# Kernel tuning notes

Hardware: AMD Instinct MI355X
Metric: run time of the kernel (lower is better)

Reference implementation:

```python
import jax, jax.numpy as jnp
import numpy as np
from jax import lax

IN_CH = 256
NUM_CLASSES = 21
ROI = 7
SCALE = 1.0 / 32
SR = 2  # sampling_ratio
B = 2
NPROP = 128
FH = FW = 32
IMG = 1024
SCORE_THRESH = 0.05
NMS_THRESH = 0.5
MAX_DET = 100


def setup_inputs() -> dict:
    key = jax.random.key(0)
    ks = jax.random.split(key, 10)
    features = jax.random.normal(ks[0], (B, IN_CH, FH, FW), jnp.float32)
    x1 = jax.random.uniform(ks[1], (B, NPROP), minval=0.0, maxval=IMG - 160.0)
    y1 = jax.random.uniform(ks[2], (B, NPROP), minval=0.0, maxval=IMG - 160.0)
    w = jax.random.uniform(ks[3], (B, NPROP), minval=32.0, maxval=160.0)
    h = jax.random.uniform(ks[4], (B, NPROP), minval=32.0, maxval=160.0)
    proposals = jnp.stack([x1, y1, x1 + w, y1 + h], axis=-1)  # [B, NPROP, 4]
    img_sizes = jnp.full((B, 2), IMG, dtype=jnp.int32)  # (h, w)
    feat_dim = IN_CH * ROI * ROI

    def kaiming(k, shape):
        return jax.random.normal(k, shape, jnp.float32) * np.float32(np.sqrt(2.0 / shape[1]))

    W1 = kaiming(ks[5], (1024, feat_dim)); b1 = jnp.zeros((1024,), jnp.float32)
    W2 = kaiming(ks[6], (1024, 1024)); b2 = jnp.zeros((1024,), jnp.float32)
    Wc = jax.random.normal(ks[7], (NUM_CLASSES, 1024), jnp.float32) * 0.01
    bc = jnp.zeros((NUM_CLASSES,), jnp.float32)
    Wb = jax.random.normal(ks[8], (NUM_CLASSES * 4, 1024), jnp.float32) * 0.001
    bb = jnp.zeros((NUM_CLASSES * 4,), jnp.float32)
    return dict(features=features, proposals=proposals, img_sizes=img_sizes,
                W1=W1, b1=b1, W2=W2, b2=b2, Wc=Wc, bc=bc, Wb=Wb, bb=bb)


def roi_align(features, bidx, rois):
    """torchvision-style RoIAlign (aligned=False), spatial_scale=SCALE, sampling_ratio=SR.
    features [B,C,H,W], bidx [N] int, rois [N,4] -> [N, C*ROI*ROI] (channel-major flatten)."""
    Bf, C, H, W = features.shape
    x1 = rois[:, 0] * SCALE; y1 = rois[:, 1] * SCALE
    x2 = rois[:, 2] * SCALE; y2 = rois[:, 3] * SCALE
    rw = jnp.maximum(x2 - x1, 1.0); rh = jnp.maximum(y2 - y1, 1.0)
    bw = rw / ROI; bh = rh / ROI
    # per-bin sample offsets: [ROI, SR]
    g = jnp.arange(ROI, dtype=jnp.float32)[:, None] + (jnp.arange(SR, dtype=jnp.float32)[None, :] + 0.5) / SR
    ys = y1[:, None, None] + g[None] * bh[:, None, None]  # [N, ROI, SR]
    xs = x1[:, None, None] + g[None] * bw[:, None, None]  # [N, ROI, SR]
    y = ys[:, :, :, None, None]  # [N,ph,sy,1,1]
    x = xs[:, None, None, :, :]  # [N,1,1,pw,sx]
    inb = (y >= -1.0) & (y <= H) & (x >= -1.0) & (x <= W)  # [N,ph,sy,pw,sx]
    yc = jnp.clip(y, 0.0, H - 1.0); xc = jnp.clip(x, 0.0, W - 1.0)
    y0f = jnp.floor(yc); x0f = jnp.floor(xc)
    y0 = y0f.astype(jnp.int32); x0 = x0f.astype(jnp.int32)
    y1i = jnp.minimum(y0 + 1, H - 1); x1i = jnp.minimum(x0 + 1, W - 1)
    ly = yc - y0f; lx = xc - x0f
    hy = 1.0 - ly; hx = 1.0 - lx
    b = bidx[:, None, None, None, None]
    # gather four corners: advanced indices broadcast -> [N,ph,sy,pw,sx,C]
    f00 = features[b, :, y0, x0]
    f01 = features[b, :, y0, x1i]
    f10 = features[b, :, y1i, x0]
    f11 = features[b, :, y1i, x1i]
    val = ((hy * hx)[..., None] * f00 + (hy * lx)[..., None] * f01
           + (ly * hx)[..., None] * f10 + (ly * lx)[..., None] * f11)
    val = val * inb[..., None]
    pooled = val.mean(axis=(2, 4))            # [N, ph, pw, C]
    pooled = jnp.transpose(pooled, (0, 3, 1, 2))  # [N, C, ph, pw] (torch layout)
    return pooled.reshape(pooled.shape[0], -1)


def decode_boxes(deltas, props):
    pw = props[..., 2] - props[..., 0]
    ph = props[..., 3] - props[..., 1]
    px = props[..., 0] + pw / 2
    py = props[..., 1] + ph / 2
    cx = px + deltas[..., 0] * pw
    cy = py + deltas[..., 1] * ph
    w = pw * jnp.exp(deltas[..., 2])
    h = ph * jnp.exp(deltas[..., 3])
    return jnp.stack([cx - w / 2, cy - h / 2, cx + w / 2, cy + h / 2], axis=-1)


def nms_fixed(boxes, scores, valid, iou_thresh, max_out):
    """Greedy NMS with fixed shapes. Returns (indices[max_out], ok_mask[max_out])."""
    M = scores.shape[0]
    s = jnp.where(valid, scores, -jnp.inf)
    order = jnp.argsort(-s)
    b = boxes[order]; v = valid[order]
    bx1, by1, bx2, by2 = b[:, 0], b[:, 1], b[:, 2], b[:, 3]
    area = (bx2 - bx1) * (by2 - by1)
    idxs = jnp.arange(M)

    def body(i, keep):
        xi1 = jnp.maximum(bx1[i], bx1); yi1 = jnp.maximum(by1[i], by1)
        xi2 = jnp.minimum(bx2[i], bx2); yi2 = jnp.minimum(by2[i], by2)
        inter = jnp.maximum(xi2 - xi1, 0.0) * jnp.maximum(yi2 - yi1, 0.0)
        iou = inter / (area[i] + area - inter + 1e-9)
        suppress = (iou > iou_thresh) & (idxs > i)
        return jnp.where(keep[i], keep & ~suppress, keep)

    keep = lax.fori_loop(0, M, body, v)
    pos = jnp.where(keep, idxs, M)
    take = jnp.sort(pos)[:max_out]
    ok = take < M
    take = jnp.where(ok, take, 0)
    return order[take], ok


def postprocess_image(probs, reg, props, img_hw):
    Ncls = probs.shape[1]
    scores = probs[:, 1:]                    # [N, C-1] (skip background)
    deltas = reg[:, 1:, :]                   # [N, C-1, 4]
    boxes = decode_boxes(deltas, props[:, None, :])  # [N, C-1, 4]
    h = img_hw[0].astype(boxes.dtype); w = img_hw[1].astype(boxes.dtype)
    boxes = jnp.stack([jnp.clip(boxes[..., 0], 0.0, w), jnp.clip(boxes[..., 1], 0.0, h),
                       jnp.clip(boxes[..., 2], 0.0, w), jnp.clip(boxes[..., 3], 0.0, h)], axis=-1)
    labels = jnp.broadcast_to(jnp.arange(1, Ncls, dtype=jnp.int32)[None, :], scores.shape)
    fb = boxes.reshape(-1, 4); fs = scores.reshape(-1); fl = labels.reshape(-1)
    valid = fs > SCORE_THRESH
    maxc = jnp.max(jnp.where(valid, jnp.max(fb, axis=1), 0.0))
    off = fl.astype(fb.dtype) * (maxc + 1.0)
    zero = jnp.zeros_like(off)
    fb_off = fb + jnp.stack([off, zero, off, zero], axis=-1)
    idx, ok = nms_fixed(fb_off, fs, valid, NMS_THRESH, MAX_DET)
    m = ok.astype(fb.dtype)
    return fb[idx] * m[:, None], fs[idx] * m, fl[idx] * ok.astype(jnp.int32)


def reference(features, proposals, img_sizes, W1, b1, W2, b2, Wc, bc, Wb, bb):
    Bn, NP = proposals.shape[0], proposals.shape[1]
    bidx = jnp.repeat(jnp.arange(Bn, dtype=jnp.int32), NP)
    props_flat = proposals.reshape(-1, 4)
    roi_feats = roi_align(features, bidx, props_flat)       # [N, C*49]
    x = jax.nn.relu(roi_feats @ W1.T + b1)
    x = jax.nn.relu(x @ W2.T + b2)
    cls_logits = x @ Wc.T + bc                              # [N, NUM_CLASSES]
    box_reg = (x @ Wb.T + bb).reshape(-1, NUM_CLASSES, 4)   # [N, NUM_CLASSES, 4]
    probs = jax.nn.softmax(cls_logits, axis=-1)
    out_b, out_s, out_l = [], [], []
    for i in range(Bn):
        p = probs[i * NP:(i + 1) * NP]
        r = box_reg[i * NP:(i + 1) * NP]
        bi, si, li = postprocess_image(p, r, proposals[i], img_sizes[i])
        out_b.append(bi); out_s.append(si); out_l.append(li)
    return jnp.stack(out_b), jnp.stack(out_s), jnp.stack(out_l)
```

## Files before the change

kernel.cpp:

```cpp
#include <hip/hip_runtime.h>
#include <math.h>

#define IN_CH   256
#define NCLS    21
#define ROIW    7
#define NPROP   128
#define BATCH   2
#define NROI    (BATCH*NPROP)
#define FEAT_DIM (IN_CH*ROIW*ROIW)
#define HID     1024
#define NCAND   (NPROP*(NCLS-1))
#define MAXDET  100
#define SCORE_T 0.05f
#define NMS_T   0.5f
#define SPLIT1  32

__global__ __launch_bounds__(256) void transpose_feat(const float* __restrict__ feat,
                                                      float* __restrict__ ft) {
    int img = blockIdx.z;
    int cb = blockIdx.y;
    int pb = blockIdx.x;
    __shared__ float t[32][33];
    int tx = threadIdx.x & 31, ty = threadIdx.x >> 5;
#pragma unroll
    for (int i = 0; i < 4; ++i) {
        int c = ty + i * 8;
        t[c][tx] = feat[(size_t)img * 262144 + (size_t)(cb * 32 + c) * 1024 + pb * 32 + tx];
    }
    __syncthreads();
#pragma unroll
    for (int i = 0; i < 4; ++i) {
        int p = ty + i * 8;
        ft[(size_t)img * 262144 + (size_t)(pb * 32 + p) * 256 + cb * 32 + tx] = t[tx][p];
    }
}

__global__ __launch_bounds__(256) void roi_align_tr(const float* __restrict__ ft,
                                                    const float* __restrict__ props,
                                                    float* __restrict__ out) {
    int n = blockIdx.x >> 1;
    int half = blockIdx.x & 1;
    int img = n / NPROP;
    int q0 = half ? 25 : 0;
    int nq = half ? 24 : 25;
    const float* pr = props + n * 4;
    float x1 = pr[0] * 0.03125f, y1 = pr[1] * 0.03125f;
    float x2 = pr[2] * 0.03125f, y2 = pr[3] * 0.03125f;
    float rw = fmaxf(x2 - x1, 1.0f), rh = fmaxf(y2 - y1, 1.0f);
    float bw = rw / 7.0f, bh = rh / 7.0f;
    int cg = threadIdx.x & 63;
    int qg = threadIdx.x >> 6;
    __shared__ float tile[25][260];
    const float* base = ft + (size_t)img * 262144 + cg * 4;
    for (int j = qg; j < nq; j += 4) {
        int q = q0 + j;
        int iy = q / 7, ix = q % 7;
        float ax = 0.f, ay = 0.f, az = 0.f, aw = 0.f;
#pragma unroll
        for (int s = 0; s < 4; ++s) {
            int sy = s >> 1, sx = s & 1;
            float gy = (float)iy + ((float)sy + 0.5f) / 2.0f;
            float gx = (float)ix + ((float)sx + 0.5f) / 2.0f;
            float y = y1 + gy * bh;
            float x = x1 + gx * bw;
            bool inb = (y >= -1.0f) && (y <= 32.0f) && (x >= -1.0f) && (x <= 32.0f);
            float yc = fminf(fmaxf(y, 0.0f), 31.0f);
            float xc = fminf(fmaxf(x, 0.0f), 31.0f);
            float y0f = floorf(yc), x0f = floorf(xc);
            int y0 = (int)y0f, x0i = (int)x0f;
            int y1i = min(y0 + 1, 31), x1i = min(x0i + 1, 31);
            float ly = yc - y0f, lx = xc - x0f;
            float hy = 1.0f - ly, hx = 1.0f - lx;
            float wg = inb ? 1.0f : 0.0f;
            float w00 = hy * hx * wg, w01 = hy * lx * wg, w10 = ly * hx * wg, w11 = ly * lx * wg;
            float4 f00 = *(const float4*)(base + (size_t)(y0 * 32 + x0i) * 256);
            float4 f01 = *(const float4*)(base + (size_t)(y0 * 32 + x1i) * 256);
            float4 f10 = *(const float4*)(base + (size_t)(y1i * 32 + x0i) * 256);
            float4 f11 = *(const float4*)(base + (size_t)(y1i * 32 + x1i) * 256);
            ax += w00 * f00.x + w01 * f01.x + w10 * f10.x + w11 * f11.x;
            ay += w00 * f00.y + w01 * f01.y + w10 * f10.y + w11 * f11.y;
            az += w00 * f00.z + w01 * f01.z + w10 * f10.z + w11 * f11.z;
            aw += w00 * f00.w + w01 * f01.w + w10 * f10.w + w11 * f11.w;
        }
        *(float4*)&tile[j][cg * 4] = make_float4(ax * 0.25f, ay * 0.25f, az * 0.25f, aw * 0.25f);
    }
    __syncthreads();
    float* ob = out + (size_t)n * FEAT_DIM + q0;
    int tid = threadIdx.x;
    if (half == 0) {
        for (int i = tid; i < 256 * 25; i += 256) {
            int c = i / 25, ql = i % 25;
            ob[c * 49 + ql] = tile[ql][c];
        }
    } else {
        for (int i = tid; i < 256 * 24; i += 256) {
            int c = i / 24, ql = i % 24;
            ob[c * 49 + ql] = tile[ql][c];
        }
    }
}

#define GBM 128
#define GBN 128
#define GBK 8
__global__ __launch_bounds__(256, 2) void gemm_tn_part(const float* __restrict__ A,
                                                       const float* __restrict__ Wt,
                                                       float* __restrict__ Cp,
                                                       int Nr, int Mo, int K) {
    const int S = gridDim.z;
    const int kchunk = K / S;
    const int k0 = blockIdx.z * kchunk;
    const int n0 = blockIdx.y * GBM;
    const int j0 = blockIdx.x * GBN;
    __shared__ float As[GBK][GBM + 4];
    __shared__ float Ws[GBK][GBN + 4];
    const int tid = threadIdx.x;
    const int tx = tid & 15;
    const int ty = tid >> 4;
    const int r0 = ty << 2;
    const int c0 = tx << 2;
    const int srow = tid >> 1;
    const int skk  = (tid & 1) << 2;
    float acc[8][8];
#pragma unroll
    for (int r = 0; r < 8; ++r)
#pragma unroll
        for (int c = 0; c < 8; ++c) acc[r][c] = 0.0f;

    const int iters = kchunk / GBK;
    const float* Abase = A + (size_t)(n0 + srow) * K + skk;
    const float* Wbase = Wt + (size_t)(j0 + srow) * K + skk;
    float4 pa = *(const float4*)(Abase + k0);
    float4 pw = *(const float4*)(Wbase + k0);

#pragma unroll 1
    for (int it = 0; it < iters; ++it) {
        __syncthreads();
        As[skk + 0][srow] = pa.x; As[skk + 1][srow] = pa.y;
        As[skk + 2][srow] = pa.z; As[skk + 3][srow] = pa.w;
        Ws[skk + 0][srow] = pw.x; Ws[skk + 1][srow] = pw.y;
        Ws[skk + 2][srow] = pw.z; Ws[skk + 3][srow] = pw.w;
        __syncthreads();
        if (it + 1 < iters) {
            int kc = k0 + (it + 1) * GBK;
            pa = *(const float4*)(Abase + kc);
            pw = *(const float4*)(Wbase + kc);
        }
        float4 fa0[2], fa1[2], fw0[2], fw1[2];
        fa0[0] = *(const float4*)&As[0][r0];
        fa1[0] = *(const float4*)&As[0][r0 + 64];
        fw0[0] = *(const float4*)&Ws[0][c0];
        fw1[0] = *(const float4*)&Ws[0][c0 + 64];
#pragma unroll
        for (int k = 0; k < GBK; ++k) {
            const int cur = k & 1, nxt = cur ^ 1;
            if (k + 1 < GBK) {
                fa0[nxt] = *(const float4*)&As[k + 1][r0];
                fa1[nxt] = *(const float4*)&As[k + 1][r0 + 64];
                fw0[nxt] = *(const float4*)&Ws[k + 1][c0];
                fw1[nxt] = *(const float4*)&Ws[k + 1][c0 + 64];
            }
            float a[8] = {fa0[cur].x, fa0[cur].y, fa0[cur].z, fa0[cur].w,
                          fa1[cur].x, fa1[cur].y, fa1[cur].z, fa1[cur].w};
            float w[8] = {fw0[cur].x, fw0[cur].y, fw0[cur].z, fw0[cur].w,
                          fw1[cur].x, fw1[cur].y, fw1[cur].z, fw1[cur].w};
#pragma unroll
            for (int r = 0; r < 8; ++r)
#pragma unroll
                for (int c = 0; c < 8; ++c)
                    acc[r][c] = fmaf(a[r], w[c], acc[r][c]);
        }
    }
#pragma unroll
    for (int r = 0; r < 8; ++r) {
        int gr = n0 + ((r < 4) ? (r0 + r) : (r0 + 64 + r - 4));
        float* o = Cp + ((size_t)blockIdx.z * Nr + gr) * Mo + j0;
        *(float4*)(o + c0)      = make_float4(acc[r][0], acc[r][1], acc[r][2], acc[r][3]);
        *(float4*)(o + c0 + 64) = make_float4(acc[r][4], acc[r][5], acc[r][6], acc[r][7]);
    }
}

__global__ __launch_bounds__(256) void reduce_bias_relu(const float* __restrict__ Cp,
                                                        const float* __restrict__ bias,
                                                        float* __restrict__ X,
                                                        int Nr, int Mo, int S) {
    int idx = blockIdx.x * 256 + threadIdx.x;
    int total = (Nr * Mo) >> 2;
    if (idx >= total) return;
    int e = idx << 2;
    int j = e % Mo;
    float4 s = make_float4(0.f, 0.f, 0.f, 0.f);
    for (int ss = 0; ss < S; ++ss) {
        float4 c = *(const float4*)(Cp + (size_t)ss * Nr * Mo + e);
        s.x += c.x; s.y += c.y; s.z += c.z; s.w += c.w;
    }
    float4 b = *(const float4*)(bias + j);
    s.x = fmaxf(s.x + b.x, 0.f); s.y = fmaxf(s.y + b.y, 0.f);
    s.z = fmaxf(s.z + b.z, 0.f); s.w = fmaxf(s.w + b.w, 0.f);
    *(float4*)(X + e) = s;
}

__global__ __launch_bounds__(256) void heads_cand_k(const float* __restrict__ Cp2,
                                                    const float* __restrict__ b2,
                                                    const float* __restrict__ Wc, const float* __restrict__ bc,
                                                    const float* __restrict__ Wb, const float* __restrict__ bb,
                                                    const float* __restrict__ props,
                                                    const int* __restrict__ img_sizes,
                                                    float* __restrict__ cbox,
                                                    float* __restrict__ csc,
                                                    unsigned long long* __restrict__ ckey,
                                                    int* __restrict__ vcount) {
    int n = blockIdx.x;
    int tid = threadIdx.x;
    if (n == 0 && tid < 2) vcount[tid] = 0;
    __shared__ float xs[HID];
    __shared__ float lg[NCLS];
    __shared__ float bs[84];
    __shared__ float ssum;
    {
        int e = n * HID + tid * 4;
        float4 s = make_float4(0.f, 0.f, 0.f, 0.f);
#pragma unroll
        for (int ss = 0; ss < 16; ++ss) {
            float4 c = *(const float4*)(Cp2 + (size_t)ss * (NROI * HID) + e);
            s.x += c.x; s.y += c.y; s.z += c.z; s.w += c.w;
        }
        float4 b = *(const float4*)(b2 + tid * 4);
        s.x = fmaxf(s.x + b.x, 0.f); s.y = fmaxf(s.y + b.y, 0.f);
        s.z = fmaxf(s.z + b.z, 0.f); s.w = fmaxf(s.w + b.w, 0.f);
        *(float4*)&xs[tid * 4] = s;
    }
    __syncthreads();
    int wave = tid >> 6, lane = tid & 63;
    for (int h = wave; h < 105; h += 4) {
        const float* w = (h < 21) ? (Wc + (size_t)h * HID) : (Wb + (size_t)(h - 21) * HID);
        float acc = 0.0f;
#pragma unroll
        for (int k0 = 0; k0 < HID; k0 += 256) {
            float4 wv = *(const float4*)(w + k0 + lane * 4);
            float4 xv = *(const float4*)&xs[k0 + lane * 4];
            acc = fmaf(wv.x, xv.x, acc);
            acc = fmaf(wv.y, xv.y, acc);
            acc = fmaf(wv.z, xv.z, acc);
            acc = fmaf(wv.w, xv.w, acc);
        }
#pragma unroll
        for (int m = 32; m; m >>= 1) acc += __shfl_xor(acc, m, 64);
        if (lane == 0) {
            if (h < 21) lg[h] = acc + bc[h];
            else bs[h - 21] = acc + bb[h - 21];
        }
    }
    __syncthreads();
    if (tid == 0) {
        float m = lg[0];
        for (int c = 1; c < 21; ++c) m = fmaxf(m, lg[c]);
        float s = 0.0f;
        for (int c = 0; c < 21; ++c) { float e = expf(lg[c] - m); lg[c] = e; s += e; }
        ssum = s;
    }
    __syncthreads();
    if (tid < 20) {
        int c = tid + 1;
        int img = n / NPROP;
        float s = lg[c] / ssum;
        const float* pr = props + n * 4;
        float pw = pr[2] - pr[0], ph = pr[3] - pr[1];
        float px = pr[0] + pw * 0.5f, py = pr[1] + ph * 0.5f;
        const float* d = &bs[c * 4];
        float cx = px + d[0] * pw;
        float cy = py + d[1] * ph;
        float w = pw * expf(d[2]);
        float h = ph * expf(d[3]);
        float bx1 = cx - w * 0.5f, by1 = cy - h * 0.5f, bx2 = cx + w * 0.5f, by2 = cy + h * 0.5f;
        float Wi = (float)img_sizes[img * 2 + 1], Hi = (float)img_sizes[img * 2 + 0];
        bx1 = fminf(fmaxf(bx1, 0.f), Wi); by1 = fminf(fmaxf(by1, 0.f), Hi);
        bx2 = fminf(fmaxf(bx2, 0.f), Wi); by2 = fminf(fmaxf(by2, 0.f), Hi);
        int t = n * 20 + tid;
        *(float4*)(cbox + (size_t)t * 4) = make_float4(bx1, by1, bx2, by2);
        csc[t] = s;
        bool valid = s > SCORE_T;
        unsigned int sb = __float_as_uint(s);
        int m = t - img * NCAND;
        ckey[t] = valid ? (((unsigned long long)sb << 32) | (unsigned int)(NCAND - 1 - m)) : 0ull;
    }
}

__global__ __launch_bounds__(256) void rank_k(const float* __restrict__ cbox,
                                              const float* __restrict__ csc,
                                              const unsigned long long* __restrict__ ckey,
                                              float* __restrict__ sbox, float* __restrict__ ssc,
                                              int* __restrict__ sm, int* __restrict__ vcount) {
    int img = blockIdx.x / 40;
    int seg = blockIdx.x % 40;
    int base = img * NCAND;
    int lm = threadIdx.x & 63;
    int chunk = threadIdx.x >> 6;
    int m = seg * 64 + lm;
    __shared__ __align__(16) unsigned long long keys[NCAND];
    for (int j = threadIdx.x; j < NCAND; j += 256) keys[j] = ckey[base + j];
    unsigned long long mykey = ckey[base + m];
    float s = csc[base + m];
    bool valid = s > SCORE_T;
    __syncthreads();
    const ulonglong2* kp = (const ulonglong2*)&keys[chunk * 640];
    int r = 0;
#pragma unroll 4
    for (int j = 0; j < 320; ++j) {
        ulonglong2 kk = kp[j];
        r += (kk.x > mykey) ? 1 : 0;
        r += (kk.y > mykey) ? 1 : 0;
    }
    __shared__ int part[4][64];
    part[chunk][lm] = r;
    __syncthreads();
    if (chunk == 0) {
        int rank = part[0][lm] + part[1][lm] + part[2][lm] + part[3][lm];
        if (valid) {
            int o = base + rank;
            *(float4*)(sbox + (size_t)o * 4) = *(const float4*)(cbox + (size_t)(base + m) * 4);
            ssc[o] = s;
            sm[o] = m;
        }
    }
    int cnt = __syncthreads_count((chunk == 0) && valid);
    if (threadIdx.x == 0) atomicAdd(&vcount[img], cnt);
}

__global__ __launch_bounds__(64) void nms_k(const int* __restrict__ sm,
                                            const float* __restrict__ sbox,
                                            const int* __restrict__ vcount,
                                            int* __restrict__ skeep) {
    int bid = blockIdx.x;
    int img = bid / 20;
    int cls = bid % 20 + 1;
    int V = vcount[img];
    __shared__ float lx1[128], ly1[128], lx2[128], ly2[128];
    __shared__ int lpos[128];
    __shared__ int lcnt;
    __shared__ int keepL[128];
    int lane = threadIdx.x;
    if (lane == 0) lcnt = 0;
    __syncthreads();
    for (int p0 = 0; p0 < V; p0 += 64) {
        int p = p0 + lane;
        bool pred = false;
        if (p < V) {
            int m = sm[img * NCAND + p];
            pred = (m % 20 + 1) == cls;
        }
        unsigned long long mask = __ballot(pred);
        int base = lcnt;
        if (pred) {
            int idx = base + __popcll(mask & ((1ull << lane) - 1ull));
            const float* bx = sbox + (size_t)(img * NCAND + (p0 + lane)) * 4;
            lx1[idx] = bx[0]; ly1[idx] = bx[1]; lx2[idx] = bx[2]; ly2[idx] = bx[3];
            lpos[idx] = p0 + lane;
        }
        __syncthreads();
        if (lane == 0) lcnt += (int)__popcll(mask);
        __syncthreads();
    }
    int C = lcnt;
    for (int j = lane; j < 128; j += 64) keepL[j] = 1;
    __syncthreads();
    for (int i = 0; i < C; ++i) {
        __syncthreads();
        if (keepL[i] == 0) continue;
        float X1 = lx1[i], Y1 = ly1[i], X2 = lx2[i], Y2 = ly2[i];
        float ai = (X2 - X1) * (Y2 - Y1);
        for (int j = i + 1 + lane; j < C; j += 64) {
            if (keepL[j]) {
                float xi1 = fmaxf(X1, lx1[j]);
                float yi1 = fmaxf(Y1, ly1[j]);
                float xi2 = fminf(X2, lx2[j]);
                float yi2 = fminf(Y2, ly2[j]);
                float inter = fmaxf(xi2 - xi1, 0.f) * fmaxf(yi2 - yi1, 0.f);
                float aj = (lx2[j] - lx1[j]) * (ly2[j] - ly1[j]);
                float iou = inter / (ai + aj - inter + 1e-9f);
                if (iou > NMS_T) keepL[j] = 0;
            }
        }
    }
    __syncthreads();
    for (int j = lane; j < C; j += 64) skeep[img * NCAND + lpos[j]] = keepL[j];
}

__global__ __launch_bounds__(256) void write_k(const float* __restrict__ sbox,
                                               const float* __restrict__ ssc,
                                               const int* __restrict__ sm,
                                               const int* __restrict__ skeep,
                                               const int* __restrict__ vcount,
                                               float* __restrict__ out) {
    int img = blockIdx.x;
    int tid = threadIdx.x;
    float* ob = out + img * MAXDET * 4;
    float* os = out + BATCH * MAXDET * 4 + img * MAXDET;
    float* ol = out + BATCH * MAXDET * 5 + img * MAXDET;
    for (int i = tid; i < MAXDET * 4; i += 256) ob[i] = 0.0f;
    for (int i = tid; i < MAXDET; i += 256) { os[i] = 0.0f; ol[i] = 0.0f; }
    __syncthreads();
    int V = vcount[img];
    int chunk = (V + 255) / 256;
    int lo = tid * chunk, hi = min(lo + chunk, V);
    int cnt = 0;
    for (int p = lo; p < hi; ++p) cnt += skeep[img * NCAND + p];
    __shared__ int cs[256];
    __shared__ int pre[256];
    cs[tid] = cnt;
    __syncthreads();
    if (tid == 0) {
        int run = 0;
        for (int t = 0; t < 256; ++t) { pre[t] = run; run += cs[t]; }
    }
    __syncthreads();
    int r = pre[tid];
    for (int p = lo; p < hi; ++p) {
        if (skeep[img * NCAND + p]) {
            if (r < MAXDET) {
                const float* bx = sbox + (size_t)(img * NCAND + p) * 4;
                ob[r * 4 + 0] = bx[0]; ob[r * 4 + 1] = bx[1];
                ob[r * 4 + 2] = bx[2]; ob[r * 4 + 3] = bx[3];
                os[r] = ssc[img * NCAND + p];
                ol[r] = (float)(sm[img * NCAND + p] % 20 + 1);
            }
            ++r;
        }
    }
}

extern "C" void kernel_launch(void* const* d_in, const int* in_sizes, int n_in,
                              void* d_out, int out_size, void* d_ws, size_t ws_size,
                              hipStream_t stream) {
    const float* features  = (const float*)d_in[0];
    const float* proposals = (const float*)d_in[1];
    const int*   img_sizes = (const int*)d_in[2];
    const float* W1 = (const float*)d_in[3];
    const float* b1 = (const float*)d_in[4];
    const float* W2 = (const float*)d_in[5];
    const float* b2 = (const float*)d_in[6];
    const float* Wc = (const float*)d_in[7];
    const float* bc = (const float*)d_in[8];
    const float* Wb = (const float*)d_in[9];
    const float* bb = (const float*)d_in[10];
    float* out = (float*)d_out;

    float* ws = (float*)d_ws;
    float* roi   = ws;
    float* x1    = roi + 3211264;
    float* cpart = x1 + 262144;
    float* featT = cpart;
    float* cbox  = cpart + (size_t)SPLIT1 * 262144;
    float* csc   = cbox + 20480;
    unsigned long long* ckey = (unsigned long long*)(csc + 5120);
    float* sbox  = csc + 5120 + 10240;
    float* ssc   = sbox + 20480;
    int*   sm    = (int*)(ssc + 5120);
    int*   skeep = sm + 5120;
    int*   vcnt  = skeep + 5120;

    hipLaunchKernelGGL(transpose_feat, dim3(32, 8, 2), dim3(256), 0, stream, features, featT);
    hipLaunchKernelGGL(roi_align_tr, dim3(NROI * 2), dim3(256), 0, stream, featT, proposals, roi);
    hipLaunchKernelGGL(gemm_tn_part, dim3(8, 2, SPLIT1), dim3(256), 0, stream, roi, W1, cpart, NROI, HID, FEAT_DIM);
    hipLaunchKernelGGL(reduce_bias_relu, dim3(256), dim3(256), 0, stream, cpart, b1, x1, NROI, HID, SPLIT1);
    hipLaunchKernelGGL(gemm_tn_part, dim3(8, 2, 16), dim3(256), 0, stream, x1, W2, cpart, NROI, HID, HID);
    hipLaunchKernelGGL(heads_cand_k, dim3(NROI), dim3(256), 0, stream, cpart, b2, Wc, bc, Wb, bb,
                       proposals, img_sizes, cbox, csc, ckey, vcnt);
    hipLaunchKernelGGL(rank_k, dim3(80), dim3(256), 0, stream, cbox, csc, ckey, sbox, ssc, sm, vcnt);
    hipLaunchKernelGGL(nms_k, dim3(BATCH * 20), dim3(64), 0, stream, sm, sbox, vcnt, skeep);
    hipLaunchKernelGGL(write_k, dim3(BATCH), dim3(256), 0, stream, sbox, ssc, sm, skeep, vcnt, out);
}
```

Baseline: 319.2 us.

## Transpose RoI features to K-major and read A operand directly into registers in FC1 GEMM

Adds a transpose kernel that writes the RoI-aligned features in K-major layout ([FEAT_DIM][NROI]). A new FC1 GEMM then loads the A tile straight from global memory into registers as coalesced float4 reads and stages only the weight tile in shared memory. This removes A staging through LDS and one barrier-bound copy per k-step. In exchange it adds an extra pass over the roughly 12.8 MB RoI feature buffer, one more kernel launch, and more register pressure from the prefetched A values.

```diff
diff --git a/kernel.cpp b/kernel.cpp
--- a/kernel.cpp
+++ b/kernel.cpp
@@ -100,9 +100,105 @@
     }
 }
 
+__global__ __launch_bounds__(256) void transpose_A(const float* __restrict__ A,
+                                                   float* __restrict__ At) {
+    __shared__ float t[32][33];
+    int fb = blockIdx.x;
+    int nb = blockIdx.y;
+    int tx = threadIdx.x & 31, ty = threadIdx.x >> 5;
+#pragma unroll
+    for (int i = 0; i < 4; ++i) {
+        int r = ty + i * 8;
+        t[r][tx] = A[(size_t)(nb * 32 + r) * FEAT_DIM + fb * 32 + tx];
+    }
+    __syncthreads();
+#pragma unroll
+    for (int i = 0; i < 4; ++i) {
+        int f = ty + i * 8;
+        At[(size_t)(fb * 32 + f) * NROI + nb * 32 + tx] = t[tx][f];
+    }
+}
+
 #define GBM 128
 #define GBN 128
 #define GBK 8
+__global__ __launch_bounds__(256, 2) void gemm_fc1(const float* __restrict__ At,
+                                                   const float* __restrict__ Wt,
+                                                   float* __restrict__ Cp,
+                                                   int Nr, int Mo, int K) {
+    const int S = gridDim.z;
+    const int kchunk = K / S;
+    const int k0 = blockIdx.z * kchunk;
+    const int n0 = blockIdx.y * GBM;
+    const int j0 = blockIdx.x * GBN;
+    __shared__ float Ws[GBK][GBN + 4];
+    const int tid = threadIdx.x;
+    const int tx = tid & 15;
+    const int ty = tid >> 4;
+    const int r0 = ty << 2;
+    const int c0 = tx << 2;
+    const int srow = tid >> 1;
+    const int skk  = (tid & 1) << 2;
+    float acc[8][8];
+#pragma unroll
+    for (int r = 0; r < 8; ++r)
+#pragma unroll
+        for (int c = 0; c < 8; ++c) acc[r][c] = 0.0f;
+
+    const int iters = kchunk / GBK;
+    const float* Wbase = Wt + (size_t)(j0 + srow) * K + skk;
+    const float* A0 = At + (size_t)k0 * Nr + n0 + r0;
+    float4 pw = *(const float4*)(Wbase + k0);
+    float4 ra0[GBK], ra1[GBK];
+#pragma unroll
+    for (int k = 0; k < GBK; ++k) {
+        ra0[k] = *(const float4*)(A0 + (size_t)k * Nr);
+        ra1[k] = *(const float4*)(A0 + (size_t)k * Nr + 64);
+    }
+
+#pragma unroll 1
+    for (int it = 0; it < iters; ++it) {
+        __syncthreads();
+        Ws[skk + 0][srow] = pw.x; Ws[skk + 1][srow] = pw.y;
+        Ws[skk + 2][srow] = pw.z; Ws[skk + 3][srow] = pw.w;
+        __syncthreads();
+        const bool more = (it + 1 < iters);
+        if (more) pw = *(const float4*)(Wbase + k0 + (it + 1) * GBK);
+        const float* Anext = A0 + (size_t)(it + 1) * GBK * Nr;
+        float4 fw0[2], fw1[2];
+        fw0[0] = *(const float4*)&Ws[0][c0];
+        fw1[0] = *(const float4*)&Ws[0][c0 + 64];
+#pragma unroll
+        for (int k = 0; k < GBK; ++k) {
+            const int cur = k & 1, nxt = cur ^ 1;
+            if (k + 1 < GBK) {
+                fw0[nxt] = *(const float4*)&Ws[k + 1][c0];
+                fw1[nxt] = *(const float4*)&Ws[k + 1][c0 + 64];
+            }
+            float a[8] = {ra0[k].x, ra0[k].y, ra0[k].z, ra0[k].w,
+                          ra1[k].x, ra1[k].y, ra1[k].z, ra1[k].w};
+            float w[8] = {fw0[cur].x, fw0[cur].y, fw0[cur].z, fw0[cur].w,
+                          fw1[cur].x, fw1[cur].y, fw1[cur].z, fw1[cur].w};
+#pragma unroll
+            for (int r = 0; r < 8; ++r)
+#pragma unroll
+                for (int c = 0; c < 8; ++c)
+                    acc[r][c] = fmaf(a[r], w[c], acc[r][c]);
+            if (more) {
+                ra0[k] = *(const float4*)(Anext + (size_t)k * Nr);
+                ra1[k] = *(const float4*)(Anext + (size_t)k * Nr + 64);
+            }
+        }
+    }
+#pragma unroll
+    for (int r = 0; r < 8; ++r) {
+        int gr = n0 + ((r < 4) ? (r0 + r) : (r0 + 64 + r - 4));
+        float* o = Cp + ((size_t)blockIdx.z * Nr + gr) * Mo + j0;
+        *(float4*)(o + c0)      = make_float4(acc[r][0], acc[r][1], acc[r][2], acc[r][3]);
+        *(float4*)(o + c0 + 64) = make_float4(acc[r][4], acc[r][5], acc[r][6], acc[r][7]);
+    }
+}
+
 __global__ __launch_bounds__(256, 2) void gemm_tn_part(const float* __restrict__ A,
                                                        const float* __restrict__ Wt,
                                                        float* __restrict__ Cp,
@@ -447,7 +543,8 @@
 
     float* ws = (float*)d_ws;
     float* roi   = ws;
-    float* x1    = roi + 3211264;
+    float* roiT  = roi + 3211264;
+    float* x1    = roiT + 3211264;
     float* cpart = x1 + 262144;
     float* featT = cpart;
     float* cbox  = cpart + (size_t)SPLIT1 * 262144;
@@ -461,7 +558,8 @@
 
     hipLaunchKernelGGL(transpose_feat, dim3(32, 8, 2), dim3(256), 0, stream, features, featT);
     hipLaunchKernelGGL(roi_align_tr, dim3(NROI * 2), dim3(256), 0, stream, featT, proposals, roi);
-    hipLaunchKernelGGL(gemm_tn_part, dim3(8, 2, SPLIT1), dim3(256), 0, stream, roi, W1, cpart, NROI, HID, FEAT_DIM);
+    hipLaunchKernelGGL(transpose_A, dim3(392, 8), dim3(256), 0, stream, roi, roiT);
+    hipLaunchKernelGGL(gemm_fc1, dim3(8, 2, SPLIT1), dim3(256), 0, stream, roiT, W1, cpart, NROI, HID, FEAT_DIM);
     hipLaunchKernelGGL(reduce_bias_relu, dim3(256), dim3(256), 0, stream, cpart, b1, x1, NROI, HID, SPLIT1);
     hipLaunchKernelGGL(gemm_tn_part, dim3(8, 2, 16), dim3(256), 0, stream, x1, W2, cpart, NROI, HID, HID);
     hipLaunchKernelGGL(heads_cand_k, dim3(NROI), dim3(256), 0, stream, cpart, b2, Wc, bc, Wb, bb,
```

New measurement: 462.5 us. +44.9%, slower.

## Fuse rank, NMS and output write into one per-image kernel; parallelize split-K reduce

Applied to the files above, without the earlier changes.

Replaces the separate rank, per-class NMS and compaction kernels with a single 1024-thread block per image. It keeps keys, per-class boxes and keep flags in shared memory and uses a parallel prefix scan. This removes launches and global round-trips for intermediate keep and count buffers, but runs the tail on only two blocks. The split-K bias+ReLU reduce now uses four threads per output combined with wave shuffles, to expose more memory parallelism.

```diff
diff --git a/kernel.cpp b/kernel.cpp
--- a/kernel.cpp
+++ b/kernel.cpp
@@ -184,20 +184,32 @@
                                                         const float* __restrict__ bias,
                                                         float* __restrict__ X,
                                                         int Nr, int Mo, int S) {
-    int idx = blockIdx.x * 256 + threadIdx.x;
-    int total = (Nr * Mo) >> 2;
-    if (idx >= total) return;
-    int e = idx << 2;
+    int gid = blockIdx.x * 256 + threadIdx.x;
+    int total4 = (Nr * Mo) >> 2;
+    int e4 = gid >> 2;
+    int part = gid & 3;
+    if (e4 >= total4) return;
+    int e = e4 << 2;
     int j = e % Mo;
+    int q = S >> 2;
     float4 s = make_float4(0.f, 0.f, 0.f, 0.f);
-    for (int ss = 0; ss < S; ++ss) {
+    for (int ss = part * q; ss < (part + 1) * q; ++ss) {
         float4 c = *(const float4*)(Cp + (size_t)ss * Nr * Mo + e);
         s.x += c.x; s.y += c.y; s.z += c.z; s.w += c.w;
     }
-    float4 b = *(const float4*)(bias + j);
-    s.x = fmaxf(s.x + b.x, 0.f); s.y = fmaxf(s.y + b.y, 0.f);
-    s.z = fmaxf(s.z + b.z, 0.f); s.w = fmaxf(s.w + b.w, 0.f);
-    *(float4*)(X + e) = s;
+#pragma unroll
+    for (int m = 1; m < 4; m <<= 1) {
+        s.x += __shfl_xor(s.x, m, 64);
+        s.y += __shfl_xor(s.y, m, 64);
+        s.z += __shfl_xor(s.z, m, 64);
+        s.w += __shfl_xor(s.w, m, 64);
+    }
+    if (part == 0) {
+        float4 b = *(const float4*)(bias + j);
+        s.x = fmaxf(s.x + b.x, 0.f); s.y = fmaxf(s.y + b.y, 0.f);
+        s.z = fmaxf(s.z + b.z, 0.f); s.w = fmaxf(s.w + b.w, 0.f);
+        *(float4*)(X + e) = s;
+    }
 }
 
 __global__ __launch_bounds__(256) void heads_cand_k(const float* __restrict__ Cp2,
@@ -208,11 +220,9 @@
                                                     const int* __restrict__ img_sizes,
                                                     float* __restrict__ cbox,
                                                     float* __restrict__ csc,
-                                                    unsigned long long* __restrict__ ckey,
-                                                    int* __restrict__ vcount) {
+                                                    unsigned long long* __restrict__ ckey) {
     int n = blockIdx.x;
     int tid = threadIdx.x;
-    if (n == 0 && tid < 2) vcount[tid] = 0;
     __shared__ float xs[HID];
     __shared__ float lg[NCLS];
     __shared__ float bs[84];
@@ -286,143 +296,124 @@
     }
 }
 
-__global__ __launch_bounds__(256) void rank_k(const float* __restrict__ cbox,
-                                              const float* __restrict__ csc,
-                                              const unsigned long long* __restrict__ ckey,
-                                              float* __restrict__ sbox, float* __restrict__ ssc,
-                                              int* __restrict__ sm, int* __restrict__ vcount) {
-    int img = blockIdx.x / 40;
-    int seg = blockIdx.x % 40;
-    int base = img * NCAND;
-    int lm = threadIdx.x & 63;
-    int chunk = threadIdx.x >> 6;
-    int m = seg * 64 + lm;
-    __shared__ __align__(16) unsigned long long keys[NCAND];
-    for (int j = threadIdx.x; j < NCAND; j += 256) keys[j] = ckey[base + j];
-    unsigned long long mykey = ckey[base + m];
-    float s = csc[base + m];
-    bool valid = s > SCORE_T;
-    __syncthreads();
-    const ulonglong2* kp = (const ulonglong2*)&keys[chunk * 640];
-    int r = 0;
+__global__ __launch_bounds__(1024) void tail_k(const float* __restrict__ cbox,
+                                               const float* __restrict__ csc,
+                                               const unsigned long long* __restrict__ ckey,
+                                               float* __restrict__ sbox,
+                                               float* __restrict__ ssc,
+                                               int* __restrict__ smg,
+                                               float* __restrict__ out) {
+    const int img = blockIdx.x;
+    const int tid = threadIdx.x;
+    const int base = img * NCAND;
+
+    __shared__ union {
+        unsigned long long keys[NCAND];
+        struct { float x1[20][128], y1[20][128], x2[20][128], y2[20][128]; } c;
+    } u;
+    __shared__ short cpos[20][128];
+    __shared__ unsigned char ckeepA[20][128];
+    __shared__ unsigned char smcls[NCAND];
+    __shared__ unsigned char keepS[NCAND];
+    __shared__ int Vs;
+    __shared__ int scanA[1024], scanB[1024];
+
+    if (tid == 0) Vs = 0;
+    for (int j2 = tid; j2 < NCAND; j2 += 1024) u.keys[j2] = ckey[base + j2];
+    __syncthreads();
+
+    int myV = 0;
+    for (int m = tid; m < NCAND; m += 1024) {
+        float s = csc[base + m];
+        if (s > SCORE_T) {
+            unsigned long long mykey = u.keys[m];
+            const ulonglong2* kp = (const ulonglong2*)u.keys;
+            int r = 0;
 #pragma unroll 4
-    for (int j = 0; j < 320; ++j) {
-        ulonglong2 kk = kp[j];
-        r += (kk.x > mykey) ? 1 : 0;
-        r += (kk.y > mykey) ? 1 : 0;
-    }
-    __shared__ int part[4][64];
-    part[chunk][lm] = r;
-    __syncthreads();
-    if (chunk == 0) {
-        int rank = part[0][lm] + part[1][lm] + part[2][lm] + part[3][lm];
-        if (valid) {
-            int o = base + rank;
+            for (int j2 = 0; j2 < NCAND / 2; ++j2) {
+                ulonglong2 kk = kp[j2];
+                r += (kk.x > mykey) ? 1 : 0;
+                r += (kk.y > mykey) ? 1 : 0;
+            }
+            int o = base + r;
             *(float4*)(sbox + (size_t)o * 4) = *(const float4*)(cbox + (size_t)(base + m) * 4);
             ssc[o] = s;
-            sm[o] = m;
-        }
-    }
-    int cnt = __syncthreads_count((chunk == 0) && valid);
-    if (threadIdx.x == 0) atomicAdd(&vcount[img], cnt);
-}
-
-__global__ __launch_bounds__(64) void nms_k(const int* __restrict__ sm,
-                                            const float* __restrict__ sbox,
-                                            const int* __restrict__ vcount,
-                                            int* __restrict__ skeep) {
-    int bid = blockIdx.x;
-    int img = bid / 20;
-    int cls = bid % 20 + 1;
-    int V = vcount[img];
-    __shared__ float lx1[128], ly1[128], lx2[128], ly2[128];
-    __shared__ int lpos[128];
-    __shared__ int lcnt;
-    __shared__ int keepL[128];
-    int lane = threadIdx.x;
-    if (lane == 0) lcnt = 0;
-    __syncthreads();
-    for (int p0 = 0; p0 < V; p0 += 64) {
-        int p = p0 + lane;
-        bool pred = false;
-        if (p < V) {
-            int m = sm[img * NCAND + p];
-            pred = (m % 20 + 1) == cls;
-        }
-        unsigned long long mask = __ballot(pred);
-        int base = lcnt;
-        if (pred) {
-            int idx = base + __popcll(mask & ((1ull << lane) - 1ull));
-            const float* bx = sbox + (size_t)(img * NCAND + (p0 + lane)) * 4;
-            lx1[idx] = bx[0]; ly1[idx] = bx[1]; lx2[idx] = bx[2]; ly2[idx] = bx[3];
-            lpos[idx] = p0 + lane;
-        }
-        __syncthreads();
-        if (lane == 0) lcnt += (int)__popcll(mask);
-        __syncthreads();
-    }
-    int C = lcnt;
-    for (int j = lane; j < 128; j += 64) keepL[j] = 1;
-    __syncthreads();
-    for (int i = 0; i < C; ++i) {
-        __syncthreads();
-        if (keepL[i] == 0) continue;
-        float X1 = lx1[i], Y1 = ly1[i], X2 = lx2[i], Y2 = ly2[i];
-        float ai = (X2 - X1) * (Y2 - Y1);
-        for (int j = i + 1 + lane; j < C; j += 64) {
-            if (keepL[j]) {
-                float xi1 = fmaxf(X1, lx1[j]);
-                float yi1 = fmaxf(Y1, ly1[j]);
-                float xi2 = fminf(X2, lx2[j]);
-                float yi2 = fminf(Y2, ly2[j]);
-                float inter = fmaxf(xi2 - xi1, 0.f) * fmaxf(yi2 - yi1, 0.f);
-                float aj = (lx2[j] - lx1[j]) * (ly2[j] - ly1[j]);
-                float iou = inter / (ai + aj - inter + 1e-9f);
-                if (iou > NMS_T) keepL[j] = 0;
+            smg[o] = m;
+            ++myV;
+        }
+    }
+    atomicAdd(&Vs, myV);
+    __syncthreads();
+    const int V = Vs;
+    for (int p = tid; p < V; p += 1024) smcls[p] = (unsigned char)(smg[base + p] % 20);
+    __syncthreads();
+
+    const int wv = tid >> 6, lane = tid & 63;
+    for (int ci = wv; ci < 20; ci += 16) {
+        int cnt = 0;
+        for (int p0 = 0; p0 < V; p0 += 64) {
+            int p = p0 + lane;
+            bool pred = (p < V) && (smcls[p] == (unsigned char)ci);
+            unsigned long long mask = __ballot(pred);
+            if (pred) {
+                int idx = cnt + (int)__popcll(mask & ((1ull << lane) - 1ull));
+                const float* bx = sbox + (size_t)(base + p) * 4;
+                u.c.x1[ci][idx] = bx[0]; u.c.y1[ci][idx] = bx[1];
+                u.c.x2[ci][idx] = bx[2]; u.c.y2[ci][idx] = bx[3];
+                cpos[ci][idx] = (short)p;
             }
-        }
-    }
-    __syncthreads();
-    for (int j = lane; j < C; j += 64) skeep[img * NCAND + lpos[j]] = keepL[j];
-}
-
-__global__ __launch_bounds__(256) void write_k(const float* __restrict__ sbox,
-                                               const float* __restrict__ ssc,
-                                               const int* __restrict__ sm,
-                                               const int* __restrict__ skeep,
-                                               const int* __restrict__ vcount,
-                                               float* __restrict__ out) {
-    int img = blockIdx.x;
-    int tid = threadIdx.x;
+            cnt += (int)__popcll(mask);
+        }
+        for (int j2 = lane; j2 < 128; j2 += 64) ckeepA[ci][j2] = 1;
+        for (int i = 0; i < cnt; ++i) {
+            if (ckeepA[ci][i] == 0) continue;
+            float X1 = u.c.x1[ci][i], Y1 = u.c.y1[ci][i];
+            float X2 = u.c.x2[ci][i], Y2 = u.c.y2[ci][i];
+            float ai = (X2 - X1) * (Y2 - Y1);
+            for (int j2 = i + 1 + lane; j2 < cnt; j2 += 64) {
+                if (ckeepA[ci][j2]) {
+                    float xi1 = fmaxf(X1, u.c.x1[ci][j2]);
+                    float yi1 = fmaxf(Y1, u.c.y1[ci][j2]);
+                    float xi2 = fminf(X2, u.c.x2[ci][j2]);
+                    float yi2 = fminf(Y2, u.c.y2[ci][j2]);
+                    float inter = fmaxf(xi2 - xi1, 0.f) * fmaxf(yi2 - yi1, 0.f);
+                    float aj = (u.c.x2[ci][j2] - u.c.x1[ci][j2]) * (u.c.y2[ci][j2] - u.c.y1[ci][j2]);
+                    float iou = inter / (ai + aj - inter + 1e-9f);
+                    if (iou > NMS_T) ckeepA[ci][j2] = 0;
+                }
+            }
+        }
+        for (int j2 = lane; j2 < cnt; j2 += 64) keepS[cpos[ci][j2]] = ckeepA[ci][j2];
+    }
+    __syncthreads();
+
     float* ob = out + img * MAXDET * 4;
     float* os = out + BATCH * MAXDET * 4 + img * MAXDET;
     float* ol = out + BATCH * MAXDET * 5 + img * MAXDET;
-    for (int i = tid; i < MAXDET * 4; i += 256) ob[i] = 0.0f;
-    for (int i = tid; i < MAXDET; i += 256) { os[i] = 0.0f; ol[i] = 0.0f; }
-    __syncthreads();
-    int V = vcount[img];
-    int chunk = (V + 255) / 256;
+    for (int i = tid; i < MAXDET * 4; i += 1024) ob[i] = 0.0f;
+    for (int i = tid; i < MAXDET; i += 1024) { os[i] = 0.0f; ol[i] = 0.0f; }
+    int chunk = (V + 1023) >> 10;
     int lo = tid * chunk, hi = min(lo + chunk, V);
-    int cnt = 0;
-    for (int p = lo; p < hi; ++p) cnt += skeep[img * NCAND + p];
-    __shared__ int cs[256];
-    __shared__ int pre[256];
-    cs[tid] = cnt;
-    __syncthreads();
-    if (tid == 0) {
-        int run = 0;
-        for (int t = 0; t < 256; ++t) { pre[t] = run; run += cs[t]; }
-    }
-    __syncthreads();
-    int r = pre[tid];
+    int cnt2 = 0;
+    for (int p = lo; p < hi; ++p) cnt2 += keepS[p];
+    scanA[tid] = cnt2;
+    __syncthreads();
+    int* src = scanA; int* dst = scanB;
+    for (int off = 1; off < 1024; off <<= 1) {
+        int v = src[tid] + ((tid >= off) ? src[tid - off] : 0);
+        dst[tid] = v;
+        __syncthreads();
+        int* t = src; src = dst; dst = t;
+    }
+    int r = (tid > 0) ? src[tid - 1] : 0;
     for (int p = lo; p < hi; ++p) {
-        if (skeep[img * NCAND + p]) {
+        if (keepS[p]) {
             if (r < MAXDET) {
-                const float* bx = sbox + (size_t)(img * NCAND + p) * 4;
+                const float* bx = sbox + (size_t)(base + p) * 4;
                 ob[r * 4 + 0] = bx[0]; ob[r * 4 + 1] = bx[1];
                 ob[r * 4 + 2] = bx[2]; ob[r * 4 + 3] = bx[3];
-                os[r] = ssc[img * NCAND + p];
-                ol[r] = (float)(sm[img * NCAND + p] % 20 + 1);
+                os[r] = ssc[base + p];
+                ol[r] = (float)(smg[base + p] % 20 + 1);
             }
             ++r;
         }
@@ -455,18 +446,14 @@
     unsigned long long* ckey = (unsigned long long*)(csc + 5120);
     float* sbox  = csc + 5120 + 10240;
     float* ssc   = sbox + 20480;
-    int*   sm    = (int*)(ssc + 5120);
-    int*   skeep = sm + 5120;
-    int*   vcnt  = skeep + 5120;
+    int*   smg   = (int*)(ssc + 5120);
 
     hipLaunchKernelGGL(transpose_feat, dim3(32, 8, 2), dim3(256), 0, stream, features, featT);
     hipLaunchKernelGGL(roi_align_tr, dim3(NROI * 2), dim3(256), 0, stream, featT, proposals, roi);
     hipLaunchKernelGGL(gemm_tn_part, dim3(8, 2, SPLIT1), dim3(256), 0, stream, roi, W1, cpart, NROI, HID, FEAT_DIM);
-    hipLaunchKernelGGL(reduce_bias_relu, dim3(256), dim3(256), 0, stream, cpart, b1, x1, NROI, HID, SPLIT1);
+    hipLaunchKernelGGL(reduce_bias_relu, dim3(1024), dim3(256), 0, stream, cpart, b1, x1, NROI, HID, SPLIT1);
     hipLaunchKernelGGL(gemm_tn_part, dim3(8, 2, 16), dim3(256), 0, stream, x1, W2, cpart, NROI, HID, HID);
     hipLaunchKernelGGL(heads_cand_k, dim3(NROI), dim3(256), 0, stream, cpart, b2, Wc, bc, Wb, bb,
-                       proposals, img_sizes, cbox, csc, ckey, vcnt);
-    hipLaunchKernelGGL(rank_k, dim3(80), dim3(256), 0, stream, cbox, csc, ckey, sbox, ssc, sm, vcnt);
-    hipLaunchKernelGGL(nms_k, dim3(BATCH * 20), dim3(64), 0, stream, sm, sbox, vcnt, skeep);
-    hipLaunchKernelGGL(write_k, dim3(BATCH), dim3(256), 0, stream, sbox, ssc, sm, skeep, vcnt, out);
-}
+                       proposals, img_sizes, cbox, csc, ckey);
+    hipLaunchKernelGGL(tail_k, dim3(BATCH), dim3(1024), 0, stream, cbox, csc, ckey, sbox, ssc, smg, out);
+}
```

New measurement: 412.3 us. 1.29x slower.
